# Kernel tuning notes

Hardware: AMD Instinct MI355X
Metric: run time of the kernel (lower is better)

## Reference

```python
import jax, jax.numpy as jnp
import numpy as np

NUM_HEADS = 12
SEG_HEADS = 6  # first 6 heads -> full attention; rest -> 4-way strided
HEAD_DIM = 64


def setup_inputs() -> dict:
    key = jax.random.key(0)
    ks = jax.random.split(key, 7)
    B, S, H = 2, 4096, 768
    sc = 0.02
    return {
        "hidden_states": jax.random.normal(ks[0], (B, S, H), jnp.float32),
        "Wq": jax.random.normal(ks[1], (H, H), jnp.float32) * sc,
        "bq": jax.random.normal(ks[2], (H,), jnp.float32) * sc,
        "Wk": jax.random.normal(ks[3], (H, H), jnp.float32) * sc,
        "bk": jax.random.normal(ks[4], (H,), jnp.float32) * sc,
        "Wv": jax.random.normal(ks[5], (H, H), jnp.float32) * sc,
        "bv": jax.random.normal(ks[6], (H,), jnp.float32) * sc,
    }


def _heads(x, B, S):
    # [B,S,H] -> [B,nH,S,D]
    return x.reshape(B, S, NUM_HEADS, HEAD_DIM).transpose(0, 2, 1, 3)


def reference(hidden_states, Wq, bq, Wk, bk, Wv, bv):
    B, S, H = hidden_states.shape
    scale = 1.0 / jnp.sqrt(jnp.float32(HEAD_DIM))

    q = _heads(hidden_states @ Wq.T + bq, B, S)
    k = _heads(hidden_states @ Wk.T + bk, B, S)
    v = _heads(hidden_states @ Wv.T + bv, B, S)

    # ---- full attention on first SEG_HEADS heads ----
    qf, kf, vf = q[:, :SEG_HEADS], k[:, :SEG_HEADS], v[:, :SEG_HEADS]
    scores = jnp.einsum('bhqd,bhkd->bhqk', qf, kf) * scale
    z_full = jnp.einsum('bhqk,bhkd->bhqd', jax.nn.softmax(scores, axis=-1), vf)

    # ---- 4-way strided attention on remaining heads ----
    # x[:,:,i::4,:] == reshape(B,h,S//4,4,D)[..., i, :]; batch the 4 groups.
    S4 = S // 4
    def strided(x):
        # [B,h,S,D] -> [B,h,4,S//4,D], group g holds positions g::4
        return x[:, SEG_HEADS:].reshape(B, NUM_HEADS - SEG_HEADS, S4, 4, HEAD_DIM).transpose(0, 1, 3, 2, 4)
    qa, ka, va = strided(q), strided(k), strided(v)
    s_ax = jnp.einsum('bhgqd,bhgkd->bhgqk', qa, ka) * scale
    z_ax = jnp.einsum('bhgqk,bhgkd->bhgqd', jax.nn.softmax(s_ax, axis=-1), va)
    # re-interleave: torch.stack(dim=3).view -> position s*4+g from (g,s)
    z_axis = z_ax.transpose(0, 1, 3, 2, 4).reshape(B, NUM_HEADS - SEG_HEADS, S, HEAD_DIM)

    ctx = jnp.concatenate([z_full, z_axis], axis=1)           # [B,nH,S,D]
    ctx = ctx.transpose(0, 2, 1, 3).reshape(B, S, NUM_HEADS * HEAD_DIM)
    return ctx
```

## Files before the change

kernel.cpp:

```cpp
#include <hip/hip_runtime.h>
#include <stdint.h>
#include <math.h>

#define BB 2
#define SS 4096
#define NHEADS 12
#define DHEAD 64

#define N_HS (8192*768)
#define N_W  (768*768)

typedef __bf16 bf16x8 __attribute__((ext_vector_type(8)));
typedef float  f32x4  __attribute__((ext_vector_type(4)));
typedef float  f32x16 __attribute__((ext_vector_type(16)));

__device__ __forceinline__ unsigned short f2bf(float x) {
  union { float f; uint32_t u; } v; v.f = x;
  uint32_t r = v.u + 0x7fffu + ((v.u >> 16) & 1u);
  return (unsigned short)(r >> 16);
}

__device__ __forceinline__ float fexp2(float x) {
#if __has_builtin(__builtin_amdgcn_exp2f)
  return __builtin_amdgcn_exp2f(x);
#else
  return exp2f(x);
#endif
}

__device__ __forceinline__ unsigned int pk_trunc(float lo, float hi) {
#if __has_builtin(__builtin_amdgcn_perm)
  return __builtin_amdgcn_perm(__float_as_uint(hi), __float_as_uint(lo), 0x07060302u);
#else
  return (__float_as_uint(hi) & 0xffff0000u) | (__float_as_uint(lo) >> 16);
#endif
}

__device__ __forceinline__ void gld16(const unsigned short* g, unsigned short* l) {
  __builtin_amdgcn_global_load_lds(
      (const __attribute__((address_space(1))) unsigned int*)g,
      (__attribute__((address_space(3))) unsigned int*)l, 16, 0, 0);
}

__global__ __launch_bounds__(256) void convert_kernel(
    const float* __restrict__ hs, const float* __restrict__ wq,
    const float* __restrict__ wk, const float* __restrict__ wv,
    unsigned short* __restrict__ hs_bf, unsigned short* __restrict__ w_bf)
{
  int i = blockIdx.x * 256 + threadIdx.x;
  const int total4 = (N_HS + 3 * N_W) / 4;
  if (i >= total4) return;
  int e = i * 4;
  const float* src; int rel; unsigned short* dst; int dofs;
  if (e < N_HS) { src = hs; rel = e; dst = hs_bf; dofs = e; }
  else {
    int r = e - N_HS; dst = w_bf; dofs = r;
    if      (r < N_W)     { src = wq; rel = r; }
    else if (r < 2 * N_W) { src = wk; rel = r - N_W; }
    else                  { src = wv; rel = r - 2 * N_W; }
  }
  float4 v = *(const float4*)(src + rel);
  union { unsigned short s[4]; uint2 u; } o;
  o.s[0] = f2bf(v.x); o.s[1] = f2bf(v.y); o.s[2] = f2bf(v.z); o.s[3] = f2bf(v.w);
  *(uint2*)(dst + dofs) = o.u;
}

__global__ __launch_bounds__(256) void qkv_gemm(
    const unsigned short* __restrict__ hs,
    const unsigned short* __restrict__ w_all,
    const float* __restrict__ bq, const float* __restrict__ bk, const float* __restrict__ bv,
    unsigned short* __restrict__ qh,
    unsigned short* __restrict__ kh,
    unsigned short* __restrict__ vt)
{
  __shared__ __align__(16) unsigned short SM[2 * 128 * 64];
  unsigned short* At = SM;
  unsigned short* Bt = SM + 128 * 64;

  const int bid = blockIdx.x;
  const int xcd = bid & 7;
  const int t   = bid >> 3;
  const int st  = (t / 48) * 8 + xcd;
  const int inner = t % 48;
  const int which = st >> 3;
  const int mbase = (st & 7) * 1024 + (inner & 7) * 128;
  const int nb    = (inner >> 3) * 128;

  const int tid = threadIdx.x;
  const unsigned short* w = w_all + (size_t)which * (768 * 768);
  const int lane = tid & 63, wid = tid >> 6;
  const int ln = lane & 15, qd = lane >> 4;
  const int wm = wid >> 1, wn = wid & 1;

  const int srow = lane >> 3;
  const int sslot = (lane & 7) ^ srow;

  f32x4 acc[4][4];
#pragma unroll
  for (int i = 0; i < 4; i++)
#pragma unroll
    for (int j = 0; j < 4; j++) acc[i][j] = (f32x4){0.f, 0.f, 0.f, 0.f};

  for (int kb = 0; kb < 12; ++kb) {
    const int kbase = kb * 64;
    __syncthreads();
#pragma unroll
    for (int j = 0; j < 4; ++j) {
      int c = wid * 4 + j;
      int row = c * 8 + srow;
      gld16(hs + (size_t)(mbase + row) * 768 + kbase + sslot * 8, &At[c * 512]);
      gld16(w  + (size_t)(nb    + row) * 768 + kbase + sslot * 8, &Bt[c * 512]);
    }
    __syncthreads();
#pragma unroll
    for (int ks = 0; ks < 2; ++ks) {
      bf16x8 af[4], bfr[4];
#pragma unroll
      for (int t2 = 0; t2 < 4; t2++) {
        int ra = wm * 64 + t2 * 16 + ln;
        int rb = wn * 64 + t2 * 16 + ln;
        int slot = (qd + 4 * ks);
        af[t2]  = *(const bf16x8*)(&At[ra * 64 + ((slot ^ (ra & 7)) * 8)]);
        bfr[t2] = *(const bf16x8*)(&Bt[rb * 64 + ((slot ^ (rb & 7)) * 8)]);
      }
#pragma unroll
      for (int i = 0; i < 4; i++)
#pragma unroll
        for (int j = 0; j < 4; j++)
          acc[i][j] = __builtin_amdgcn_mfma_f32_16x16x32_bf16(af[i], bfr[j], acc[i][j], 0, 0, 0);
    }
  }

  const float* bias = (which == 0) ? bq : (which == 1) ? bk : bv;
  const float postscale = (which == 0) ? 0.18033688011112042f : 1.0f;
  const int n0 = nb + wn * 64;
  const int hh = n0 >> 6;
  const int mrow0 = mbase + wm * 64;
  const int bgl = mrow0 >> 12;
  const int s0 = mrow0 & 4095;
  const bool axisv = (which == 2) && (hh >= 6);

  __syncthreads();
  unsigned short* T = SM + wid * 4096;

  if (which < 2) {
#pragma unroll
    for (int j = 0; j < 4; j++) {
      float bb = bias[n0 + j * 16 + ln];
#pragma unroll
      for (int i = 0; i < 4; i++)
#pragma unroll
        for (int r = 0; r < 4; r++)
          T[(i * 16 + qd * 4 + r) * 64 + j * 16 + ln] =
              f2bf((acc[i][j][r] + bb) * postscale);
    }
  } else if (!axisv) {
#pragma unroll
    for (int j = 0; j < 4; j++) {
      float bb = bias[n0 + j * 16 + ln];
#pragma unroll
      for (int i = 0; i < 4; i++) {
        unsigned int p01 = (unsigned int)f2bf(acc[i][j][0] + bb) |
                           ((unsigned int)f2bf(acc[i][j][1] + bb) << 16);
        unsigned int p23 = (unsigned int)f2bf(acc[i][j][2] + bb) |
                           ((unsigned int)f2bf(acc[i][j][3] + bb) << 16);
        int base = (j * 16 + ln) * 64 + i * 16 + qd * 4;
        *(unsigned int*)(&T[base])     = p01;
        *(unsigned int*)(&T[base + 2]) = p23;
      }
    }
  } else {
#pragma unroll
    for (int j = 0; j < 4; j++) {
      float bb = bias[n0 + j * 16 + ln];
#pragma unroll
      for (int i = 0; i < 4; i++)
#pragma unroll
        for (int r = 0; r < 4; r++)
          T[(j * 16 + ln) * 64 + r * 16 + i * 4 + qd] = f2bf(acc[i][j][r] + bb);
    }
  }
  __syncthreads();

  if (which < 2) {
    unsigned short* dp = ((which == 0) ? qh : kh) +
                         ((size_t)(bgl * 12 + hh) * 4096 + s0) * 64;
#pragma unroll
    for (int c = 0; c < 8; ++c) {
      int lin = c * 64 + lane;
      int row = lin >> 3, sl8 = (lin & 7) * 8;
      *(uint4*)(dp + row * 64 + sl8) = *(const uint4*)(&T[row * 64 + sl8]);
    }
  } else if (!axisv) {
    unsigned short* dp = vt + (size_t)(bgl * 12 + hh) * 64 * 4096 + s0;
#pragma unroll
    for (int c = 0; c < 8; ++c) {
      int lin = c * 64 + lane;
      int drow = lin >> 3, sl8 = (lin & 7) * 8;
      *(uint4*)(dp + (size_t)drow * 4096 + sl8) = *(const uint4*)(&T[drow * 64 + sl8]);
    }
  } else {
    const int i0_0 = s0 >> 2;
    unsigned short* dp = vt + (size_t)(bgl * 12 + hh) * 64 * 4096;
#pragma unroll
    for (int c = 0; c < 8; ++c) {
      int lin = c * 64 + lane;
      int drow = lin >> 3, sl = lin & 7;
      int g = sl >> 1, io = (sl & 1) * 8;
      *(uint4*)(dp + (size_t)drow * 4096 + g * 1024 + i0_0 + io) =
          *(const uint4*)(&T[drow * 64 + sl * 8]);
    }
  }
}

__device__ __forceinline__ void make_frags(const unsigned int* P, int hi,
                                           bf16x8* fa, bf16x8* fb) {
  unsigned int s0 = hi ? P[0] : P[2];
  unsigned int s1 = hi ? P[1] : P[3];
  unsigned int r0 = (unsigned int)__shfl_xor((int)s0, 32, 64);
  unsigned int r1 = (unsigned int)__shfl_xor((int)s1, 32, 64);
  unsigned int t0 = hi ? P[4] : P[6];
  unsigned int t1 = hi ? P[5] : P[7];
  unsigned int u0 = (unsigned int)__shfl_xor((int)t0, 32, 64);
  unsigned int u1 = (unsigned int)__shfl_xor((int)t1, 32, 64);
  union { unsigned int u[4]; bf16x8 v; } A, B;
  A.u[0] = hi ? r0 : P[0];
  A.u[1] = hi ? r1 : P[1];
  A.u[2] = hi ? P[2] : r0;
  A.u[3] = hi ? P[3] : r1;
  B.u[0] = hi ? u0 : P[4];
  B.u[1] = hi ? u1 : P[5];
  B.u[2] = hi ? P[6] : u0;
  B.u[3] = hi ? P[7] : u1;
  *fa = A.v; *fb = B.v;
}

__global__ __launch_bounds__(256) void attn_kernel(
    const unsigned short* __restrict__ qh,
    const unsigned short* __restrict__ kh,
    const unsigned short* __restrict__ vt,
    float* __restrict__ out,
    float* __restrict__ PO, float* __restrict__ PL)
{
  __shared__ __align__(16) unsigned short Kt[2 * 64 * 72];
  __shared__ __align__(16) unsigned short Vt[2 * 64 * 72];

  const int bid = blockIdx.x;
  int b, h, g, qt, nkt, kt0, strided, half, bh;
  if (bid < 768) {
    int xcd = bid & 7, t = bid >> 3;
    int gb = t >> 5; qt = t & 31;
    int gfull = gb * 8 + xcd;
    bh = gfull >> 1; half = gfull & 1;
    b = bh / 6; h = bh % 6;
    g = 0; strided = 0; nkt = 32; kt0 = half * 32;
  } else {
    int r = bid - 768;
    int xcd = r & 7, t = r >> 3;
    int gb = t >> 3; qt = t & 7;
    int g2 = gb * 8 + xcd;
    int bhi = g2 >> 2; g = g2 & 3;
    b = bhi / 6; h = 6 + bhi % 6;
    strided = 1; nkt = 16; kt0 = 0; half = 0; bh = 0;
  }
  const size_t headoff = (size_t)(b * 12 + h) * 4096 * 64;
  const unsigned short* qp = qh + headoff;
  const unsigned short* kp = kh + headoff;
  const unsigned short* vp = vt + headoff;

  const int tid = threadIdx.x;
  const int lane = tid & 63, w = tid >> 6;
  const int l32 = lane & 31, hi = lane >> 5;
  const int hi8 = hi * 8;

  const int qrow = qt * 128 + w * 32 + l32;
  const int sQ = strided ? (qrow * 4 + g) : qrow;
  bf16x8 qf[4];
#pragma unroll
  for (int c = 0; c < 4; ++c)
    qf[c] = *(const bf16x8*)(qp + (size_t)sQ * 64 + c * 16 + hi8);

  union { unsigned int u[4]; bf16x8 v; } ones_;
#pragma unroll
  for (int i = 0; i < 4; i++) ones_.u[i] = 0x3f803f80u;
  const bf16x8 onesf = ones_.v;

  const int srow0 = tid >> 3,        scol0 = (tid & 7) * 8;
  const int srow1 = (tid + 256) >> 3, scol1 = ((tid + 256) & 7) * 8;
  const int s0g = kt0 * 64 + srow0, s1g = kt0 * 64 + srow1;
  const unsigned short* kptr0 = kp + (size_t)(strided ? (s0g * 4 + g) : s0g) * 64 + scol0;
  const unsigned short* kptr1 = kp + (size_t)(strided ? (s1g * 4 + g) : s1g) * 64 + scol1;
  const int vb0 = strided ? g * 1024 : 0;
  const unsigned short* vptr0 = vp + (size_t)srow0 * 4096 + vb0 + kt0 * 64 + scol0;
  const unsigned short* vptr1 = vp + (size_t)srow1 * 4096 + vb0 + kt0 * 64 + scol1;
  const int kstep = (strided ? 256 : 64) * 64;
  const int lofs0 = srow0 * 72 + scol0, lofs1 = srow1 * 72 + scol1;

  uint4 rk0 = *(const uint4*)kptr0, rk1 = *(const uint4*)kptr1;
  uint4 rv0 = *(const uint4*)vptr0, rv1 = *(const uint4*)vptr1;
  kptr0 += kstep; kptr1 += kstep; vptr0 += 64; vptr1 += 64;
  *(uint4*)(&Kt[lofs0]) = rk0; *(uint4*)(&Kt[lofs1]) = rk1;
  *(uint4*)(&Vt[lofs0]) = rv0; *(uint4*)(&Vt[lofs1]) = rv1;
  __syncthreads();

  f32x16 o0, o1, lacc;
#pragma unroll
  for (int i = 0; i < 16; i++) { o0[i] = 0.f; o1[i] = 0.f; lacc[i] = 0.f; }

  for (int kt = 0; kt < nkt; ++kt) {
    const int cur = (kt & 1) * 4608, nxt = 4608 - cur;
    const bool pf = (kt + 1 < nkt);
    if (pf) {
      rk0 = *(const uint4*)kptr0; rk1 = *(const uint4*)kptr1;
      rv0 = *(const uint4*)vptr0; rv1 = *(const uint4*)vptr1;
      kptr0 += kstep; kptr1 += kstep; vptr0 += 64; vptr1 += 64;
    }

    f32x16 sc0, sc1;
#pragma unroll
    for (int i = 0; i < 16; i++) { sc0[i] = 0.f; sc1[i] = 0.f; }
#pragma unroll
    for (int c = 0; c < 4; ++c) {
      bf16x8 k0 = *(const bf16x8*)(&Kt[cur + l32 * 72 + c * 16 + hi8]);
      sc0 = __builtin_amdgcn_mfma_f32_32x32x16_bf16(k0, qf[c], sc0, 0, 0, 0);
      bf16x8 k1 = *(const bf16x8*)(&Kt[cur + (32 + l32) * 72 + c * 16 + hi8]);
      sc1 = __builtin_amdgcn_mfma_f32_32x32x16_bf16(k1, qf[c], sc1, 0, 0, 0);
    }

    unsigned int P0[8], P1[8];
#pragma unroll
    for (int u = 0; u < 8; ++u) {
      float a = fexp2(sc0[2 * u]);
      float c = fexp2(sc0[2 * u + 1]);
      P0[u] = pk_trunc(a, c);
    }
#pragma unroll
    for (int u = 0; u < 8; ++u) {
      float a = fexp2(sc1[2 * u]);
      float c = fexp2(sc1[2 * u + 1]);
      P1[u] = pk_trunc(a, c);
    }

    bf16x8 pfr[4];
    make_frags(P0, hi, &pfr[0], &pfr[1]);
    make_frags(P1, hi, &pfr[2], &pfr[3]);

#pragma unroll
    for (int c = 0; c < 4; ++c) {
      bf16x8 v0 = *(const bf16x8*)(&Vt[cur + l32 * 72 + c * 16 + hi8]);
      o0 = __builtin_amdgcn_mfma_f32_32x32x16_bf16(v0, pfr[c], o0, 0, 0, 0);
      bf16x8 v1 = *(const bf16x8*)(&Vt[cur + (32 + l32) * 72 + c * 16 + hi8]);
      o1 = __builtin_amdgcn_mfma_f32_32x32x16_bf16(v1, pfr[c], o1, 0, 0, 0);
      lacc = __builtin_amdgcn_mfma_f32_32x32x16_bf16(onesf, pfr[c], lacc, 0, 0, 0);
    }

    if (pf) {
      *(uint4*)(&Kt[nxt + lofs0]) = rk0; *(uint4*)(&Kt[nxt + lofs1]) = rk1;
      *(uint4*)(&Vt[nxt + lofs0]) = rv0; *(uint4*)(&Vt[nxt + lofs1]) = rv1;
    }
    __syncthreads();
  }

  const float ltot = lacc[0];
  if (!strided) {
    size_t base = ((size_t)(bh * 2 + half) * 4096 + sQ) * 64;
#pragma unroll
    for (int mt = 0; mt < 2; ++mt) {
#pragma unroll
      for (int a = 0; a < 4; ++a) {
        float4 vv;
        vv.x = mt ? o1[4 * a + 0] : o0[4 * a + 0];
        vv.y = mt ? o1[4 * a + 1] : o0[4 * a + 1];
        vv.z = mt ? o1[4 * a + 2] : o0[4 * a + 2];
        vv.w = mt ? o1[4 * a + 3] : o0[4 * a + 3];
        *(float4*)(&PO[base + mt * 32 + a * 8 + hi * 4]) = vv;
      }
    }
    if (hi == 0) PL[(bh * 2 + half) * 4096 + sQ] = ltot;
  } else {
    float inv = 1.0f / ltot;
    size_t base = ((size_t)b * 4096 + sQ) * 768 + h * 64;
#pragma unroll
    for (int mt = 0; mt < 2; ++mt) {
#pragma unroll
      for (int a = 0; a < 4; ++a) {
        float4 vv;
        vv.x = (mt ? o1[4 * a + 0] : o0[4 * a + 0]) * inv;
        vv.y = (mt ? o1[4 * a + 1] : o0[4 * a + 1]) * inv;
        vv.z = (mt ? o1[4 * a + 2] : o0[4 * a + 2]) * inv;
        vv.w = (mt ? o1[4 * a + 3] : o0[4 * a + 3]) * inv;
        *(float4*)(&out[base + mt * 32 + a * 8 + hi * 4]) = vv;
      }
    }
  }
}

__global__ __launch_bounds__(256) void merge_kernel(
    const float* __restrict__ PO, const float* __restrict__ PL,
    float* __restrict__ out)
{
  int i = blockIdx.x * 256 + threadIdx.x;
  int c4 = i & 15;
  int qrow = (i >> 4) & 4095;
  int bh = i >> 16;
  size_t p0 = (((size_t)bh * 2 + 0) * 4096 + qrow) * 64 + c4 * 4;
  size_t p1 = (((size_t)bh * 2 + 1) * 4096 + qrow) * 64 + c4 * 4;
  float4 a = *(const float4*)(&PO[p0]);
  float4 c = *(const float4*)(&PO[p1]);
  float l = PL[(bh * 2 + 0) * 4096 + qrow] + PL[(bh * 2 + 1) * 4096 + qrow];
  float inv = 1.0f / l;
  float4 o;
  o.x = (a.x + c.x) * inv; o.y = (a.y + c.y) * inv;
  o.z = (a.z + c.z) * inv; o.w = (a.w + c.w) * inv;
  int b = bh / 6, h = bh % 6;
  *(float4*)(&out[((size_t)b * 4096 + qrow) * 768 + h * 64 + c4 * 4]) = o;
}

extern "C" void kernel_launch(void* const* d_in, const int* in_sizes, int n_in,
                              void* d_out, int out_size, void* d_ws, size_t ws_size,
                              hipStream_t stream) {
  const float* hs = (const float*)d_in[0];
  const float* Wq = (const float*)d_in[1];
  const float* bq = (const float*)d_in[2];
  const float* Wk = (const float*)d_in[3];
  const float* bk = (const float*)d_in[4];
  const float* Wv = (const float*)d_in[5];
  const float* bv = (const float*)d_in[6];
  float* out = (float*)d_out;

  unsigned short* q_bf  = (unsigned short*)d_ws;
  unsigned short* k_bf  = q_bf + (size_t)BB * NHEADS * SS * DHEAD;
  unsigned short* vt_bf = k_bf + (size_t)BB * NHEADS * SS * DHEAD;
  unsigned short* hs_bf = vt_bf + (size_t)BB * NHEADS * SS * DHEAD;
  unsigned short* w_bf  = hs_bf + (size_t)N_HS;
  float* PO = (float*)hs_bf;
  float* PL = PO + (size_t)12 * 2 * 4096 * 64;

  const int total4 = (N_HS + 3 * N_W) / 4;
  convert_kernel<<<(total4 + 255) / 256, 256, 0, stream>>>(hs, Wq, Wk, Wv, hs_bf, w_bf);

  qkv_gemm<<<1152, 256, 0, stream>>>(hs_bf, w_bf, bq, bk, bv, q_bf, k_bf, vt_bf);

  attn_kernel<<<1152, 256, 0, stream>>>(q_bf, k_bf, vt_bf, out, PO, PL);

  merge_kernel<<<3072, 256, 0, stream>>>(PO, PL, out);
}
```

Baseline: 236.5 us.

## Process two query sub-tiles per warp to reuse K/V LDS fragments

Result: faster. 225.4 us (-4.7%).

```diff
diff --git a/kernel.cpp b/kernel.cpp
--- a/kernel.cpp
+++ b/kernel.cpp
@@ -235,7 +235,7 @@
   *fa = A.v; *fb = B.v;
 }
 
-__global__ __launch_bounds__(256) void attn_kernel(
+__global__ __launch_bounds__(256, 2) void attn_kernel(
     const unsigned short* __restrict__ qh,
     const unsigned short* __restrict__ kh,
     const unsigned short* __restrict__ vt,
@@ -247,17 +247,17 @@
 
   const int bid = blockIdx.x;
   int b, h, g, qt, nkt, kt0, strided, half, bh;
-  if (bid < 768) {
+  if (bid < 384) {
     int xcd = bid & 7, t = bid >> 3;
-    int gb = t >> 5; qt = t & 31;
+    int gb = t >> 4; qt = t & 15;
     int gfull = gb * 8 + xcd;
     bh = gfull >> 1; half = gfull & 1;
     b = bh / 6; h = bh % 6;
     g = 0; strided = 0; nkt = 32; kt0 = half * 32;
   } else {
-    int r = bid - 768;
+    int r = bid - 384;
     int xcd = r & 7, t = r >> 3;
-    int gb = t >> 3; qt = t & 7;
+    int gb = t >> 2; qt = t & 3;
     int g2 = gb * 8 + xcd;
     int bhi = g2 >> 2; g = g2 & 3;
     b = bhi / 6; h = 6 + bhi % 6;
@@ -273,12 +273,15 @@
   const int l32 = lane & 31, hi = lane >> 5;
   const int hi8 = hi * 8;
 
-  const int qrow = qt * 128 + w * 32 + l32;
-  const int sQ = strided ? (qrow * 4 + g) : qrow;
-  bf16x8 qf[4];
-#pragma unroll
-  for (int c = 0; c < 4; ++c)
-    qf[c] = *(const bf16x8*)(qp + (size_t)sQ * 64 + c * 16 + hi8);
+  const int qrowA = qt * 256 + w * 64 + l32;
+  const int sQA = strided ? (qrowA * 4 + g) : qrowA;
+  const int sQB = sQA + (strided ? 128 : 32);
+  bf16x8 qfA[4], qfB[4];
+#pragma unroll
+  for (int c = 0; c < 4; ++c) {
+    qfA[c] = *(const bf16x8*)(qp + (size_t)sQA * 64 + c * 16 + hi8);
+    qfB[c] = *(const bf16x8*)(qp + (size_t)sQB * 64 + c * 16 + hi8);
+  }
 
   union { unsigned int u[4]; bf16x8 v; } ones_;
 #pragma unroll
@@ -303,9 +306,12 @@
   *(uint4*)(&Vt[lofs0]) = rv0; *(uint4*)(&Vt[lofs1]) = rv1;
   __syncthreads();
 
-  f32x16 o0, o1, lacc;
-#pragma unroll
-  for (int i = 0; i < 16; i++) { o0[i] = 0.f; o1[i] = 0.f; lacc[i] = 0.f; }
+  f32x16 oA0, oA1, oB0, oB1, laccA, laccB;
+#pragma unroll
+  for (int i = 0; i < 16; i++) {
+    oA0[i] = 0.f; oA1[i] = 0.f; oB0[i] = 0.f; oB1[i] = 0.f;
+    laccA[i] = 0.f; laccB[i] = 0.f;
+  }
 
   for (int kt = 0; kt < nkt; ++kt) {
     const int cur = (kt & 1) * 4608, nxt = 4608 - cur;
@@ -316,42 +322,51 @@
       kptr0 += kstep; kptr1 += kstep; vptr0 += 64; vptr1 += 64;
     }
 
-    f32x16 sc0, sc1;
-#pragma unroll
-    for (int i = 0; i < 16; i++) { sc0[i] = 0.f; sc1[i] = 0.f; }
+    f32x16 scA0, scA1, scB0, scB1;
+#pragma unroll
+    for (int i = 0; i < 16; i++) { scA0[i] = 0.f; scA1[i] = 0.f; scB0[i] = 0.f; scB1[i] = 0.f; }
 #pragma unroll
     for (int c = 0; c < 4; ++c) {
       bf16x8 k0 = *(const bf16x8*)(&Kt[cur + l32 * 72 + c * 16 + hi8]);
-      sc0 = __builtin_amdgcn_mfma_f32_32x32x16_bf16(k0, qf[c], sc0, 0, 0, 0);
       bf16x8 k1 = *(const bf16x8*)(&Kt[cur + (32 + l32) * 72 + c * 16 + hi8]);
-      sc1 = __builtin_amdgcn_mfma_f32_32x32x16_bf16(k1, qf[c], sc1, 0, 0, 0);
-    }
-
-    unsigned int P0[8], P1[8];
-#pragma unroll
-    for (int u = 0; u < 8; ++u) {
-      float a = fexp2(sc0[2 * u]);
-      float c = fexp2(sc0[2 * u + 1]);
-      P0[u] = pk_trunc(a, c);
-    }
-#pragma unroll
-    for (int u = 0; u < 8; ++u) {
-      float a = fexp2(sc1[2 * u]);
-      float c = fexp2(sc1[2 * u + 1]);
-      P1[u] = pk_trunc(a, c);
-    }
-
-    bf16x8 pfr[4];
-    make_frags(P0, hi, &pfr[0], &pfr[1]);
-    make_frags(P1, hi, &pfr[2], &pfr[3]);
+      scA0 = __builtin_amdgcn_mfma_f32_32x32x16_bf16(k0, qfA[c], scA0, 0, 0, 0);
+      scA1 = __builtin_amdgcn_mfma_f32_32x32x16_bf16(k1, qfA[c], scA1, 0, 0, 0);
+      scB0 = __builtin_amdgcn_mfma_f32_32x32x16_bf16(k0, qfB[c], scB0, 0, 0, 0);
+      scB1 = __builtin_amdgcn_mfma_f32_32x32x16_bf16(k1, qfB[c], scB1, 0, 0, 0);
+    }
+
+    bf16x8 pfrA[4], pfrB[4];
+    {
+      unsigned int P0[8], P1[8];
+#pragma unroll
+      for (int u = 0; u < 8; ++u) {
+        P0[u] = pk_trunc(fexp2(scA0[2 * u]), fexp2(scA0[2 * u + 1]));
+        P1[u] = pk_trunc(fexp2(scA1[2 * u]), fexp2(scA1[2 * u + 1]));
+      }
+      make_frags(P0, hi, &pfrA[0], &pfrA[1]);
+      make_frags(P1, hi, &pfrA[2], &pfrA[3]);
+    }
+    {
+      unsigned int P0[8], P1[8];
+#pragma unroll
+      for (int u = 0; u < 8; ++u) {
+        P0[u] = pk_trunc(fexp2(scB0[2 * u]), fexp2(scB0[2 * u + 1]));
+        P1[u] = pk_trunc(fexp2(scB1[2 * u]), fexp2(scB1[2 * u + 1]));
+      }
+      make_frags(P0, hi, &pfrB[0], &pfrB[1]);
+      make_frags(P1, hi, &pfrB[2], &pfrB[3]);
+    }
 
 #pragma unroll
     for (int c = 0; c < 4; ++c) {
       bf16x8 v0 = *(const bf16x8*)(&Vt[cur + l32 * 72 + c * 16 + hi8]);
-      o0 = __builtin_amdgcn_mfma_f32_32x32x16_bf16(v0, pfr[c], o0, 0, 0, 0);
       bf16x8 v1 = *(const bf16x8*)(&Vt[cur + (32 + l32) * 72 + c * 16 + hi8]);
-      o1 = __builtin_amdgcn_mfma_f32_32x32x16_bf16(v1, pfr[c], o1, 0, 0, 0);
-      lacc = __builtin_amdgcn_mfma_f32_32x32x16_bf16(onesf, pfr[c], lacc, 0, 0, 0);
+      oA0 = __builtin_amdgcn_mfma_f32_32x32x16_bf16(v0, pfrA[c], oA0, 0, 0, 0);
+      oA1 = __builtin_amdgcn_mfma_f32_32x32x16_bf16(v1, pfrA[c], oA1, 0, 0, 0);
+      oB0 = __builtin_amdgcn_mfma_f32_32x32x16_bf16(v0, pfrB[c], oB0, 0, 0, 0);
+      oB1 = __builtin_amdgcn_mfma_f32_32x32x16_bf16(v1, pfrB[c], oB1, 0, 0, 0);
+      laccA = __builtin_amdgcn_mfma_f32_32x32x16_bf16(onesf, pfrA[c], laccA, 0, 0, 0);
+      laccB = __builtin_amdgcn_mfma_f32_32x32x16_bf16(onesf, pfrB[c], laccB, 0, 0, 0);
     }
 
     if (pf) {
@@ -361,35 +376,50 @@
     __syncthreads();
   }
 
-  const float ltot = lacc[0];
+  const float ltotA = laccA[0], ltotB = laccB[0];
   if (!strided) {
-    size_t base = ((size_t)(bh * 2 + half) * 4096 + sQ) * 64;
+    size_t baseA = ((size_t)(bh * 2 + half) * 4096 + sQA) * 64;
+    size_t baseB = ((size_t)(bh * 2 + half) * 4096 + sQB) * 64;
 #pragma unroll
     for (int mt = 0; mt < 2; ++mt) {
 #pragma unroll
       for (int a = 0; a < 4; ++a) {
-        float4 vv;
-        vv.x = mt ? o1[4 * a + 0] : o0[4 * a + 0];
-        vv.y = mt ? o1[4 * a + 1] : o0[4 * a + 1];
-        vv.z = mt ? o1[4 * a + 2] : o0[4 * a + 2];
-        vv.w = mt ? o1[4 * a + 3] : o0[4 * a + 3];
-        *(float4*)(&PO[base + mt * 32 + a * 8 + hi * 4]) = vv;
-      }
-    }
-    if (hi == 0) PL[(bh * 2 + half) * 4096 + sQ] = ltot;
+        float4 va, vb;
+        va.x = mt ? oA1[4 * a + 0] : oA0[4 * a + 0];
+        va.y = mt ? oA1[4 * a + 1] : oA0[4 * a + 1];
+        va.z = mt ? oA1[4 * a + 2] : oA0[4 * a + 2];
+        va.w = mt ? oA1[4 * a + 3] : oA0[4 * a + 3];
+        vb.x = mt ? oB1[4 * a + 0] : oB0[4 * a + 0];
+        vb.y = mt ? oB1[4 * a + 1] : oB0[4 * a + 1];
+        vb.z = mt ? oB1[4 * a + 2] : oB0[4 * a + 2];
+        vb.w = mt ? oB1[4 * a + 3] : oB0[4 * a + 3];
+        *(float4*)(&PO[baseA + mt * 32 + a * 8 + hi * 4]) = va;
+        *(float4*)(&PO[baseB + mt * 32 + a * 8 + hi * 4]) = vb;
+      }
+    }
+    if (hi == 0) {
+      PL[(bh * 2 + half) * 4096 + sQA] = ltotA;
+      PL[(bh * 2 + half) * 4096 + sQB] = ltotB;
+    }
   } else {
-    float inv = 1.0f / ltot;
-    size_t base = ((size_t)b * 4096 + sQ) * 768 + h * 64;
+    float invA = 1.0f / ltotA, invB = 1.0f / ltotB;
+    size_t baseA = ((size_t)b * 4096 + sQA) * 768 + h * 64;
+    size_t baseB = ((size_t)b * 4096 + sQB) * 768 + h * 64;
 #pragma unroll
     for (int mt = 0; mt < 2; ++mt) {
 #pragma unroll
       for (int a = 0; a < 4; ++a) {
-        float4 vv;
-        vv.x = (mt ? o1[4 * a + 0] : o0[4 * a + 0]) * inv;
-        vv.y = (mt ? o1[4 * a + 1] : o0[4 * a + 1]) * inv;
-        vv.z = (mt ? o1[4 * a + 2] : o0[4 * a + 2]) * inv;
-        vv.w = (mt ? o1[4 * a + 3] : o0[4 * a + 3]) * inv;
-        *(float4*)(&out[base + mt * 32 + a * 8 + hi * 4]) = vv;
+        float4 va, vb;
+        va.x = (mt ? oA1[4 * a + 0] : oA0[4 * a + 0]) * invA;
+        va.y = (mt ? oA1[4 * a + 1] : oA0[4 * a + 1]) * invA;
+        va.z = (mt ? oA1[4 * a + 2] : oA0[4 * a + 2]) * invA;
+        va.w = (mt ? oA1[4 * a + 3] : oA0[4 * a + 3]) * invA;
+        vb.x = (mt ? oB1[4 * a + 0] : oB0[4 * a + 0]) * invB;
+        vb.y = (mt ? oB1[4 * a + 1] : oB0[4 * a + 1]) * invB;
+        vb.z = (mt ? oB1[4 * a + 2] : oB0[4 * a + 2]) * invB;
+        vb.w = (mt ? oB1[4 * a + 3] : oB0[4 * a + 3]) * invB;
+        *(float4*)(&out[baseA + mt * 32 + a * 8 + hi * 4]) = va;
+        *(float4*)(&out[baseB + mt * 32 + a * 8 + hi * 4]) = vb;
       }
     }
   }
@@ -441,7 +471,7 @@
 
   qkv_gemm<<<1152, 256, 0, stream>>>(hs_bf, w_bf, bq, bk, bv, q_bf, k_bf, vt_bf);
 
-  attn_kernel<<<1152, 256, 0, stream>>>(q_bf, k_bf, vt_bf, out, PO, PL);
+  attn_kernel<<<576, 256, 0, stream>>>(q_bf, k_bf, vt_bf, out, PO, PL);
 
   merge_kernel<<<3072, 256, 0, stream>>>(PO, PL, out);
 }
```
